# Optimization experiments

Hardware: AMD Instinct MI355X
Metric: run time of the kernel (lower is better)

Reference implementation:

```python
import jax, jax.numpy as jnp
import numpy as np

B, S, E, H = 2, 2048, 1024, 16
D = E // H  # head_dim = 64


def setup_inputs() -> dict:
    key = jax.random.key(0)
    ks = jax.random.split(key, 9)
    s = 1.0 / np.sqrt(E)
    return {
        "x": jax.random.normal(ks[0], (B, S, E), dtype=jnp.float32),
        "Wq": jax.random.uniform(ks[1], (E, E), jnp.float32, -s, s),
        "bq": jax.random.uniform(ks[2], (E,), jnp.float32, -s, s),
        "Wk": jax.random.uniform(ks[3], (E, E), jnp.float32, -s, s),
        "bk": jax.random.uniform(ks[4], (E,), jnp.float32, -s, s),
        "Wv": jax.random.uniform(ks[5], (E, E), jnp.float32, -s, s),
        "bv": jax.random.uniform(ks[6], (E,), jnp.float32, -s, s),
        "Wo": jax.random.uniform(ks[7], (E, E), jnp.float32, -s, s),
        "bo": jax.random.uniform(ks[8], (E,), jnp.float32, -s, s),
    }


def reference(x, Wq, bq, Wk, bk, Wv, bv, Wo, bo):
    # QKV projections (torch Linear: x @ W.T + b), split into heads: [B,H,S,D]
    def proj(t, W, b):
        return (t @ W.T + b).reshape(B, S, H, D).transpose(0, 2, 1, 3)

    Q = proj(x, Wq, bq)
    K = proj(x, Wk, bk)
    V = proj(x, Wv, bv)
    # scores [B,H,S,S], scaled by sqrt(head_dim)
    score = jnp.einsum('bnqd,bnkd->bnqk', Q, K) / jnp.sqrt(jnp.float32(D))
    weights = jax.nn.softmax(score, axis=-1)
    out = jnp.einsum('bnql,bnld->bnqd', weights, V)  # [B,H,S,D]
    out = out.transpose(0, 2, 1, 3).reshape(B, S, E)
    return out @ Wo.T + bo
```

## Files before the change

kernel.cpp:

```cpp
#include <hip/hip_runtime.h>


#define B_ 2
#define S_ 2048
#define E_ 1024
#define H_ 16
#define D_ 64
#define M_ (B_ * S_)

typedef __attribute__((ext_vector_type(8))) _Float16 f16x8;
typedef __attribute__((ext_vector_type(4))) _Float16 f16x4;
typedef __attribute__((ext_vector_type(4))) float f32x4;
typedef __attribute__((ext_vector_type(8))) unsigned short u16x8;

#define LOG2E 1.44269504f
#define CEXP  3.0f

static __device__ __forceinline__ float bf16_to_f32(unsigned short u) {
    return __uint_as_float(((unsigned)u) << 16);
}
static __device__ __forceinline__ unsigned short f32_to_bf16(float f) {
    unsigned u = __float_as_uint(f);
    u += 0x7FFFu + ((u >> 16) & 1u);
    return (unsigned short)(u >> 16);
}
static __device__ __forceinline__ float load1_f32(const void* p, int i, bool isbf) {
    return isbf ? bf16_to_f32(((const unsigned short*)p)[i]) : ((const float*)p)[i];
}
static __device__ __forceinline__ void store1(void* p, size_t i, float v, bool isbf) {
    if (isbf) ((unsigned short*)p)[i] = f32_to_bf16(v);
    else      ((float*)p)[i] = v;
}
static __device__ __forceinline__ void gl2lds16(const void* g, void* l) {
    __builtin_amdgcn_global_load_lds((const __attribute__((address_space(1))) unsigned int*)g,
                                     (__attribute__((address_space(3))) unsigned int*)l, 16, 0, 0);
}

__global__ void detect_dtype(const unsigned short* __restrict__ x, int* __restrict__ flag) {
    const int lane = threadIdx.x;
    const unsigned short h = x[2 * lane];
    const int e = (h >> 7) & 0xFF;
    const bool sane = (e >= 0x60 && e <= 0x9F);
    const unsigned long long m = __ballot(sane);
    if (lane == 0) *flag = (__popcll(m) >= 48) ? 1 : 0;
}

__global__ __launch_bounds__(256) void convert_inputs(
    const void* __restrict__ x,  const void* __restrict__ wq,
    const void* __restrict__ wk, const void* __restrict__ wv,
    const void* __restrict__ wo, const int* __restrict__ flag,
    _Float16* __restrict__ x16, _Float16* __restrict__ w16)
{
    const bool isbf = (*flag != 0);
    const size_t t = ((size_t)blockIdx.x * 256 + threadIdx.x) * 8;
    const void* src; size_t off; _Float16* dst; float scale = 1.0f;
    if (t < (size_t)M_ * E_) { src = x; off = t; dst = x16 + t; }
    else {
        const size_t u = t - (size_t)M_ * E_;
        const int wsel = (int)(u >> 20);
        off = u & ((1u << 20) - 1);
        src = wsel == 0 ? wq : wsel == 1 ? wk : wsel == 2 ? wv : wo;
        dst = w16 + u;
        if (wsel == 0) scale = 0.125f;
    }
    f16x8 v;
    if (isbf) {
        u16x8 s = *(const u16x8*)((const unsigned short*)src + off);
        #pragma unroll
        for (int j = 0; j < 8; ++j) v[j] = (_Float16)(bf16_to_f32(s[j]) * scale);
    } else {
        const float* f = (const float*)src + off;
        f32x4 lo = *(const f32x4*)f;
        f32x4 hi = *(const f32x4*)(f + 4);
        #pragma unroll
        for (int j = 0; j < 4; ++j) {
            v[j]     = (_Float16)(lo[j] * scale);
            v[4 + j] = (_Float16)(hi[j] * scale);
        }
    }
    *(f16x8*)dst = v;
}

__global__ __launch_bounds__(256) void gemm_qkv(
    const _Float16* __restrict__ x16, const _Float16* __restrict__ w16,
    const void* __restrict__ bq, const void* __restrict__ bk, const void* __restrict__ bv,
    const int* __restrict__ flag,
    _Float16* __restrict__ Qb, _Float16* __restrict__ Kb, _Float16* __restrict__ VTb)
{
    __shared__ __align__(16) _Float16 As[128 * 32];
    __shared__ __align__(16) _Float16 Bs[128 * 32];
    const bool isbf = (*flag != 0);
    const int tid = threadIdx.x, wave = tid >> 6, lane = tid & 63;
    const int wm = wave >> 1, wn = wave & 1;
    const int qd = lane >> 4, ln = lane & 15;
    const int m0 = blockIdx.x * 128;
    const int by = blockIdx.y;
    const int wsel = by >> 3;
    const int n0 = (by & 7) * 128;
    const _Float16* W = w16 + ((size_t)wsel << 20);

    const int i0 = wave * 64 + lane;
    const int i1 = i0 + 256;
    const _Float16* ga0 = x16 + (size_t)(m0 + (i0 >> 2)) * E_ + (i0 & 3) * 8;
    const _Float16* ga1 = x16 + (size_t)(m0 + (i1 >> 2)) * E_ + (i1 & 3) * 8;
    const _Float16* gb0 = W + (size_t)(n0 + (i0 >> 2)) * E_ + (i0 & 3) * 8;
    const _Float16* gb1 = W + (size_t)(n0 + (i1 >> 2)) * E_ + (i1 & 3) * 8;
    char* lA0 = (char*)As + (size_t)(wave * 64) * 16;
    char* lA1 = (char*)As + (size_t)(wave * 64 + 256) * 16;
    char* lB0 = (char*)Bs + (size_t)(wave * 64) * 16;
    char* lB1 = (char*)Bs + (size_t)(wave * 64 + 256) * 16;

    const _Float16* aS = (wsel == 2) ? Bs : As;
    const _Float16* bS = (wsel == 2) ? As : Bs;

    f32x4 acc[16] = {};

    for (int kt = 0; kt < E_; kt += 32) {
        __syncthreads();
        gl2lds16(ga0 + kt, lA0);
        gl2lds16(ga1 + kt, lA1);
        gl2lds16(gb0 + kt, lB0);
        gl2lds16(gb1 + kt, lB1);
        __syncthreads();
        f16x8 a[4], b[4];
        #pragma unroll
        for (int mt = 0; mt < 4; ++mt)
            a[mt] = *(const f16x8*)&aS[(wm * 64 + mt * 16 + ln) * 32 + qd * 8];
        #pragma unroll
        for (int nt = 0; nt < 4; ++nt)
            b[nt] = *(const f16x8*)&bS[(wn * 64 + nt * 16 + ln) * 32 + qd * 8];
        #pragma unroll
        for (int mt = 0; mt < 4; ++mt)
            #pragma unroll
            for (int nt = 0; nt < 4; ++nt)
                acc[mt * 4 + nt] = __builtin_amdgcn_mfma_f32_16x16x32_f16(a[mt], b[nt], acc[mt * 4 + nt], 0, 0, 0);
    }

    if (wsel != 2) {
        const void* bias = wsel == 0 ? bq : bk;
        const float bscale = (wsel == 0) ? 0.125f : 1.0f;
        _Float16* dst = wsel == 0 ? Qb : Kb;
        #pragma unroll
        for (int nt = 0; nt < 4; ++nt) {
            const int n = n0 + wn * 64 + nt * 16 + ln;
            const float bvv = load1_f32(bias, n, isbf) * bscale;
            const int h = n >> 6, d = n & 63;
            #pragma unroll
            for (int mt = 0; mt < 4; ++mt)
                #pragma unroll
                for (int r = 0; r < 4; ++r) {
                    const int m = m0 + wm * 64 + mt * 16 + qd * 4 + r;
                    const int b = m >> 11, s = m & (S_ - 1);
                    dst[((size_t)(b * H_ + h) * S_ + s) * D_ + d] =
                        (_Float16)(acc[mt * 4 + nt][r] + bvv);
                }
        }
    } else {
        #pragma unroll
        for (int mt = 0; mt < 4; ++mt)
            #pragma unroll
            for (int r = 0; r < 4; ++r) {
                const int e = n0 + wm * 64 + mt * 16 + qd * 4 + r;
                const float bvv = load1_f32(bv, e, isbf);
                const int h = e >> 6, d = e & 63;
                #pragma unroll
                for (int nt = 0; nt < 4; ++nt) {
                    const int sg = m0 + wn * 64 + nt * 16 + ln;
                    const int b = sg >> 11, s = sg & (S_ - 1);
                    VTb[((size_t)(b * H_ + h) * D_ + d) * S_ + s] =
                        (_Float16)(acc[mt * 4 + nt][r] + bvv);
                }
            }
    }
}

__global__ __launch_bounds__(256) void attn(
    const _Float16* __restrict__ Q, const _Float16* __restrict__ K,
    const _Float16* __restrict__ VT, _Float16* __restrict__ AO)
{
    __shared__ __align__(16) _Float16 Ks[2][64][72];
    __shared__ __align__(16) _Float16 Ps[128][72];

    const int tid = threadIdx.x, wave = tid >> 6, lane = tid & 63;
    const int qd = lane >> 4, ln = lane & 15;
    const int L = blockIdx.x;
    const int bh = ((L & 7) << 2) | ((L >> 3) & 3);
    const int qt = L >> 5;
    const int b = bh >> 4, h = bh & (H_ - 1);

    const _Float16* Kbase = K + (size_t)bh * S_ * D_;
    const _Float16* Vbase = VT + (size_t)bh * D_ * S_;

    f16x8 qf[2][2];
    #pragma unroll
    for (int g = 0; g < 2; ++g) {
        const _Float16* qrow = Q + ((size_t)bh * S_ + qt * 128 + wave * 32 + g * 16 + ln) * D_;
        qf[g][0] = *(const f16x8*)(qrow + qd * 8);
        qf[g][1] = *(const f16x8*)(qrow + 32 + qd * 8);
    }

    f32x4 o[2][4] = {};
    float li[2] = {0.0f, 0.0f};

    const int sr = tid >> 2, sc0 = (tid & 3) * 16;
    {
        const _Float16* src = Kbase + (size_t)sr * D_ + sc0;
        *(f16x8*)&Ks[0][sr][sc0]     = *(const f16x8*)src;
        *(f16x8*)&Ks[0][sr][sc0 + 8] = *(const f16x8*)(src + 8);
    }
    __syncthreads();

    for (int kt = 0; kt < S_; kt += 64) {
        const int p = (kt >> 6) & 1;

        f16x8 vf[2][4];
        #pragma unroll
        for (int kk = 0; kk < 2; ++kk)
            #pragma unroll
            for (int dt = 0; dt < 4; ++dt)
                vf[kk][dt] = *(const f16x8*)(Vbase + (size_t)(dt * 16 + ln) * S_ + kt + kk * 32 + qd * 8);

        const bool more = (kt + 64) < S_;
        f16x8 kn0, kn1;
        if (more) {
            const _Float16* src = Kbase + (size_t)(kt + 64) * D_ + (size_t)sr * D_ + sc0;
            kn0 = *(const f16x8*)src;
            kn1 = *(const f16x8*)(src + 8);
        }

        f16x8 af[2][4];
        #pragma unroll
        for (int kk = 0; kk < 2; ++kk)
            #pragma unroll
            for (int t4 = 0; t4 < 4; ++t4)
                af[kk][t4] = *(const f16x8*)&Ks[p][t4 * 16 + ln][kk * 32 + qd * 8];

        #pragma unroll
        for (int g = 0; g < 2; ++g) {
            f32x4 sc[4] = {};
            #pragma unroll
            for (int kk = 0; kk < 2; ++kk)
                #pragma unroll
                for (int t4 = 0; t4 < 4; ++t4)
                    sc[t4] = __builtin_amdgcn_mfma_f32_16x16x32_f16(af[kk][t4], qf[g][kk], sc[t4], 0, 0, 0);

            float ls = li[g];
            #pragma unroll
            for (int t4 = 0; t4 < 4; ++t4) {
                f16x4 ph;
                #pragma unroll
                for (int r = 0; r < 4; ++r) {
                    const float e = exp2f(fmaf(sc[t4][r], LOG2E, -CEXP * LOG2E));
                    ls += e;
                    ph[r] = (_Float16)e;
                }
                *(f16x4*)&Ps[wave * 32 + g * 16 + ln][t4 * 16 + qd * 4] = ph;
            }
            li[g] = ls;
        }

        #pragma unroll
        for (int g = 0; g < 2; ++g)
            #pragma unroll
            for (int kk = 0; kk < 2; ++kk) {
                f16x8 pf = *(const f16x8*)&Ps[wave * 32 + g * 16 + ln][kk * 32 + qd * 8];
                #pragma unroll
                for (int dt = 0; dt < 4; ++dt)
                    o[g][dt] = __builtin_amdgcn_mfma_f32_16x16x32_f16(pf, vf[kk][dt], o[g][dt], 0, 0, 0);
            }

        if (more) {
            *(f16x8*)&Ks[p ^ 1][sr][sc0]     = kn0;
            *(f16x8*)&Ks[p ^ 1][sr][sc0 + 8] = kn1;
        }
        __syncthreads();
    }

    #pragma unroll
    for (int g = 0; g < 2; ++g) {
        li[g] += __shfl_xor(li[g], 16, 64);
        li[g] += __shfl_xor(li[g], 32, 64);
    }

    #pragma unroll
    for (int g = 0; g < 2; ++g)
        #pragma unroll
        for (int r = 0; r < 4; ++r) {
            const float lr = __shfl(li[g], qd * 4 + r, 64);
            const float inv = 1.0f / lr;
            const int s = qt * 128 + wave * 32 + g * 16 + qd * 4 + r;
            #pragma unroll
            for (int dt = 0; dt < 4; ++dt)
                AO[((size_t)b * S_ + s) * E_ + h * D_ + dt * 16 + ln] = (_Float16)(o[g][dt][r] * inv);
        }
}

__global__ __launch_bounds__(256) void gemm_out(
    const _Float16* __restrict__ A, const _Float16* __restrict__ W,
    const void* __restrict__ bias, const int* __restrict__ flag, void* __restrict__ out)
{
    __shared__ __align__(16) _Float16 As[128 * 32];
    __shared__ __align__(16) _Float16 Bs[128 * 32];
    const bool isbf = (*flag != 0);
    const int tid = threadIdx.x, wave = tid >> 6, lane = tid & 63;
    const int wm = wave >> 1, wn = wave & 1;
    const int qd = lane >> 4, ln = lane & 15;
    const int m0 = blockIdx.x * 128;
    const int n0 = blockIdx.y * 128;

    const int i0 = wave * 64 + lane;
    const int i1 = i0 + 256;
    const _Float16* ga0 = A + (size_t)(m0 + (i0 >> 2)) * E_ + (i0 & 3) * 8;
    const _Float16* ga1 = A + (size_t)(m0 + (i1 >> 2)) * E_ + (i1 & 3) * 8;
    const _Float16* gb0 = W + (size_t)(n0 + (i0 >> 2)) * E_ + (i0 & 3) * 8;
    const _Float16* gb1 = W + (size_t)(n0 + (i1 >> 2)) * E_ + (i1 & 3) * 8;
    char* lA0 = (char*)As + (size_t)(wave * 64) * 16;
    char* lA1 = (char*)As + (size_t)(wave * 64 + 256) * 16;
    char* lB0 = (char*)Bs + (size_t)(wave * 64) * 16;
    char* lB1 = (char*)Bs + (size_t)(wave * 64 + 256) * 16;

    f32x4 acc[16] = {};

    for (int kt = 0; kt < E_; kt += 32) {
        __syncthreads();
        gl2lds16(ga0 + kt, lA0);
        gl2lds16(ga1 + kt, lA1);
        gl2lds16(gb0 + kt, lB0);
        gl2lds16(gb1 + kt, lB1);
        __syncthreads();
        f16x8 a[4], b[4];
        #pragma unroll
        for (int mt = 0; mt < 4; ++mt)
            a[mt] = *(const f16x8*)&As[(wm * 64 + mt * 16 + ln) * 32 + qd * 8];
        #pragma unroll
        for (int nt = 0; nt < 4; ++nt)
            b[nt] = *(const f16x8*)&Bs[(wn * 64 + nt * 16 + ln) * 32 + qd * 8];
        #pragma unroll
        for (int mt = 0; mt < 4; ++mt)
            #pragma unroll
            for (int nt = 0; nt < 4; ++nt)
                acc[mt * 4 + nt] = __builtin_amdgcn_mfma_f32_16x16x32_f16(a[mt], b[nt], acc[mt * 4 + nt], 0, 0, 0);
    }

    #pragma unroll
    for (int nt = 0; nt < 4; ++nt) {
        const int n = n0 + wn * 64 + nt * 16 + ln;
        const float bvv = load1_f32(bias, n, isbf);
        #pragma unroll
        for (int mt = 0; mt < 4; ++mt)
            #pragma unroll
            for (int r = 0; r < 4; ++r) {
                const int m = m0 + wm * 64 + mt * 16 + qd * 4 + r;
                store1(out, (size_t)m * E_ + n, acc[mt * 4 + nt][r] + bvv, isbf);
            }
    }
}

extern "C" void kernel_launch(void* const* d_in, const int* in_sizes, int n_in,
                              void* d_out, int out_size, void* d_ws, size_t ws_size,
                              hipStream_t stream) {
    const void* x  = d_in[0];
    const void* Wq = d_in[1];
    const void* bq = d_in[2];
    const void* Wk = d_in[3];
    const void* bk = d_in[4];
    const void* Wv = d_in[5];
    const void* bv = d_in[6];
    const void* Wo = d_in[7];
    const void* bo = d_in[8];

    int* flag = (int*)d_ws;
    _Float16* x16 = (_Float16*)((char*)d_ws + 1024);
    _Float16* w16 = x16 + (size_t)M_ * E_;
    _Float16* Qb  = w16 + 4u * (size_t)E_ * E_;
    _Float16* Kb  = Qb + (size_t)M_ * E_;
    _Float16* VTb = Kb + (size_t)M_ * E_;
    _Float16* AO  = x16;

    detect_dtype<<<1, 64, 0, stream>>>((const unsigned short*)x, flag);
    convert_inputs<<<4096, 256, 0, stream>>>(x, Wq, Wk, Wv, Wo, flag, x16, w16);
    gemm_qkv<<<dim3(32, 24), 256, 0, stream>>>(x16, w16, bq, bk, bv, flag, Qb, Kb, VTb);
    attn<<<512, 256, 0, stream>>>(Qb, Kb, VTb, AO);
    gemm_out<<<dim3(32, 8), 256, 0, stream>>>(AO, w16 + 3u * (size_t)E_ * E_, bo, flag, d_out);
}
```

Baseline: 228.4 us.

## Halve attention query tile per block and compute row sums with MFMA

The attention kernel now processes 64 query rows per block (16 per wave) instead of 128, doubling the grid to 1024 blocks for more parallelism and less register pressure. The softmax denominator is no longer summed on the vector ALU and reduced with cross-lane shuffles; it is accumulated by an extra MFMA of the P tile against a ones vector. In exchange, each K/V tile is loaded and staged twice as often across the grid, and the extra MFMA per step adds matrix-unit work.

```diff
diff --git a/kernel.cpp b/kernel.cpp
--- a/kernel.cpp
+++ b/kernel.cpp
@@ -179,7 +179,7 @@
     const _Float16* __restrict__ VT, _Float16* __restrict__ AO)
 {
     __shared__ __align__(16) _Float16 Ks[2][64][72];
-    __shared__ __align__(16) _Float16 Ps[128][72];
+    __shared__ __align__(16) _Float16 Ps[64][72];
 
     const int tid = threadIdx.x, wave = tid >> 6, lane = tid & 63;
     const int qd = lane >> 4, ln = lane & 15;
@@ -191,16 +191,17 @@
     const _Float16* Kbase = K + (size_t)bh * S_ * D_;
     const _Float16* Vbase = VT + (size_t)bh * D_ * S_;
 
-    f16x8 qf[2][2];
+    const _Float16* qrow = Q + ((size_t)bh * S_ + qt * 64 + wave * 16 + ln) * D_;
+    f16x8 qf[2];
+    qf[0] = *(const f16x8*)(qrow + qd * 8);
+    qf[1] = *(const f16x8*)(qrow + 32 + qd * 8);
+
+    f16x8 ones;
     #pragma unroll
-    for (int g = 0; g < 2; ++g) {
-        const _Float16* qrow = Q + ((size_t)bh * S_ + qt * 128 + wave * 32 + g * 16 + ln) * D_;
-        qf[g][0] = *(const f16x8*)(qrow + qd * 8);
-        qf[g][1] = *(const f16x8*)(qrow + 32 + qd * 8);
-    }
-
-    f32x4 o[2][4] = {};
-    float li[2] = {0.0f, 0.0f};
+    for (int j = 0; j < 8; ++j) ones[j] = (_Float16)1.0f;
+
+    f32x4 o[4] = {};
+    f32x4 liacc = {};
 
     const int sr = tid >> 2, sc0 = (tid & 3) * 16;
     {
@@ -223,51 +224,37 @@
         const bool more = (kt + 64) < S_;
         f16x8 kn0, kn1;
         if (more) {
-            const _Float16* src = Kbase + (size_t)(kt + 64) * D_ + (size_t)sr * D_ + sc0;
+            const _Float16* src = Kbase + (size_t)(kt + 64 + sr) * D_ + sc0;
             kn0 = *(const f16x8*)src;
             kn1 = *(const f16x8*)(src + 8);
         }
 
-        f16x8 af[2][4];
+        f32x4 sc[4] = {};
         #pragma unroll
         for (int kk = 0; kk < 2; ++kk)
             #pragma unroll
-            for (int t4 = 0; t4 < 4; ++t4)
-                af[kk][t4] = *(const f16x8*)&Ks[p][t4 * 16 + ln][kk * 32 + qd * 8];
-
-        #pragma unroll
-        for (int g = 0; g < 2; ++g) {
-            f32x4 sc[4] = {};
-            #pragma unroll
-            for (int kk = 0; kk < 2; ++kk)
-                #pragma unroll
-                for (int t4 = 0; t4 < 4; ++t4)
-                    sc[t4] = __builtin_amdgcn_mfma_f32_16x16x32_f16(af[kk][t4], qf[g][kk], sc[t4], 0, 0, 0);
-
-            float ls = li[g];
-            #pragma unroll
             for (int t4 = 0; t4 < 4; ++t4) {
-                f16x4 ph;
-                #pragma unroll
-                for (int r = 0; r < 4; ++r) {
-                    const float e = exp2f(fmaf(sc[t4][r], LOG2E, -CEXP * LOG2E));
-                    ls += e;
-                    ph[r] = (_Float16)e;
-                }
-                *(f16x4*)&Ps[wave * 32 + g * 16 + ln][t4 * 16 + qd * 4] = ph;
+                f16x8 a = *(const f16x8*)&Ks[p][t4 * 16 + ln][kk * 32 + qd * 8];
+                sc[t4] = __builtin_amdgcn_mfma_f32_16x16x32_f16(a, qf[kk], sc[t4], 0, 0, 0);
             }
-            li[g] = ls;
-        }
-
-        #pragma unroll
-        for (int g = 0; g < 2; ++g)
-            #pragma unroll
-            for (int kk = 0; kk < 2; ++kk) {
-                f16x8 pf = *(const f16x8*)&Ps[wave * 32 + g * 16 + ln][kk * 32 + qd * 8];
-                #pragma unroll
-                for (int dt = 0; dt < 4; ++dt)
-                    o[g][dt] = __builtin_amdgcn_mfma_f32_16x16x32_f16(pf, vf[kk][dt], o[g][dt], 0, 0, 0);
-            }
+
+        #pragma unroll
+        for (int t4 = 0; t4 < 4; ++t4) {
+            f16x4 ph;
+            #pragma unroll
+            for (int r = 0; r < 4; ++r)
+                ph[r] = (_Float16)exp2f(fmaf(sc[t4][r], LOG2E, -CEXP * LOG2E));
+            *(f16x4*)&Ps[wave * 16 + ln][t4 * 16 + qd * 4] = ph;
+        }
+
+        #pragma unroll
+        for (int kk = 0; kk < 2; ++kk) {
+            f16x8 pf = *(const f16x8*)&Ps[wave * 16 + ln][kk * 32 + qd * 8];
+            #pragma unroll
+            for (int dt = 0; dt < 4; ++dt)
+                o[dt] = __builtin_amdgcn_mfma_f32_16x16x32_f16(pf, vf[kk][dt], o[dt], 0, 0, 0);
+            liacc = __builtin_amdgcn_mfma_f32_16x16x32_f16(pf, ones, liacc, 0, 0, 0);
+        }
 
         if (more) {
             *(f16x8*)&Ks[p ^ 1][sr][sc0]     = kn0;
@@ -277,22 +264,13 @@
     }
 
     #pragma unroll
-    for (int g = 0; g < 2; ++g) {
-        li[g] += __shfl_xor(li[g], 16, 64);
-        li[g] += __shfl_xor(li[g], 32, 64);
-    }
-
-    #pragma unroll
-    for (int g = 0; g < 2; ++g)
-        #pragma unroll
-        for (int r = 0; r < 4; ++r) {
-            const float lr = __shfl(li[g], qd * 4 + r, 64);
-            const float inv = 1.0f / lr;
-            const int s = qt * 128 + wave * 32 + g * 16 + qd * 4 + r;
-            #pragma unroll
-            for (int dt = 0; dt < 4; ++dt)
-                AO[((size_t)b * S_ + s) * E_ + h * D_ + dt * 16 + ln] = (_Float16)(o[g][dt][r] * inv);
-        }
+    for (int r = 0; r < 4; ++r) {
+        const float inv = 1.0f / liacc[r];
+        const int s = qt * 64 + wave * 16 + qd * 4 + r;
+        #pragma unroll
+        for (int dt = 0; dt < 4; ++dt)
+            AO[((size_t)b * S_ + s) * E_ + h * D_ + dt * 16 + ln] = (_Float16)(o[dt][r] * inv);
+    }
 }
 
 __global__ __launch_bounds__(256) void gemm_out(
@@ -380,6 +358,6 @@
     detect_dtype<<<1, 64, 0, stream>>>((const unsigned short*)x, flag);
     convert_inputs<<<4096, 256, 0, stream>>>(x, Wq, Wk, Wv, Wo, flag, x16, w16);
     gemm_qkv<<<dim3(32, 24), 256, 0, stream>>>(x16, w16, bq, bk, bv, flag, Qb, Kb, VTb);
-    attn<<<512, 256, 0, stream>>>(Qb, Kb, VTb, AO);
+    attn<<<1024, 256, 0, stream>>>(Qb, Kb, VTb, AO);
     gemm_out<<<dim3(32, 8), 256, 0, stream>>>(AO, w16 + 3u * (size_t)E_ * E_, bo, flag, d_out);
 }
```

Result: slower. 286.2 us (+25.3%).
